# Performance work log

Measured on AMD Instinct MI355X. Metric: run time of the kernel, lower is better.

## Reference

```python
import jax, jax.numpy as jnp
import numpy as np

N, D, Q, V = 16384, 128, 16384, 64

def setup_inputs() -> dict:
    key = jax.random.key(0)
    k1, k2, k3 = jax.random.split(key, 3)
    points = jax.random.normal(k1, (N, D), dtype=jnp.float32)
    values = jax.random.normal(k2, (N, V), dtype=jnp.float32)
    points_q = jax.random.normal(k3, (Q, D), dtype=jnp.float32)
    return {"points": points, "values": values, "points_q": points_q}

def reference(points, values, points_q):
    # Squared Euclidean distances via GEMM form: |q|^2 - 2 q.p + |p|^2  -> [Q, N]
    q_sq = jnp.sum(points_q * points_q, axis=-1, keepdims=True)          # [Q, 1]
    p_sq = jnp.sum(points * points, axis=-1)                             # [N]
    dist2 = q_sq - 2.0 * jnp.einsum('qd,nd->qn', points_q, points) + p_sq
    nn_idx = jnp.argmin(dist2, axis=-1)                                  # [Q]
    return values[nn_idx]                                                # [Q, V]
```

## Files before the change

### kernel.cpp

```cpp
#include <hip/hip_runtime.h>

#define N_PTS 16384
#define DIMS  128
#define NQ    16384
#define NV    64
#define KT2   256
#define BK    64
#define BM    128
#define BN    128
#define CHUNK_NT 16
#define CHUNK_N  (BN * CHUNK_NT)
#define NCHUNK   (N_PTS / CHUNK_N)

typedef __attribute__((ext_vector_type(8))) _Float16 half8;
typedef __attribute__((ext_vector_type(4))) _Float16 half4;
typedef __attribute__((ext_vector_type(4))) float    f32x4;

#define QBLOCKS (NQ * DIMS / 1024)
#define PBLOCKS (N_PTS * DIMS / 1024)
__global__ __launch_bounds__(256) void split_fused(const float* __restrict__ q,
                                                   const float* __restrict__ pts,
                                                   _Float16* __restrict__ Aq,
                                                   _Float16* __restrict__ Bp,
                                                   float* __restrict__ p_sq,
                                                   unsigned long long* __restrict__ keys) {
    int t = blockIdx.x * 256 + threadIdx.x;
    if (t < NQ) keys[t] = ~0ull;
    const float* src;
    _Float16* dst;
    int t2;
    bool is_p = blockIdx.x >= QBLOCKS;
    if (is_p) { t2 = t - QBLOCKS * 256; src = pts; dst = Bp; }
    else      { t2 = t;                 src = q;   dst = Aq; }
    int idx4 = t2 * 4;
    int r = idx4 >> 7, c = idx4 & 127;
    float4 x = *(const float4*)(src + idx4);
    float xs[4] = {x.x, x.y, x.z, x.w};
    half4 h1, h2;
    float s = 0.f;
#pragma unroll
    for (int j = 0; j < 4; ++j) {
        _Float16 a = (_Float16)xs[j];
        h1[j] = a;
        h2[j] = (_Float16)(xs[j] - (float)a);
        s += xs[j] * xs[j];
    }
    _Float16* o = dst + (size_t)r * KT2 + c;
    *(half4*)o = h1; *(half4*)(o + 128) = h2;
    if (is_p) {
#pragma unroll
        for (int off = 1; off < 32; off <<= 1) s += __shfl_xor(s, off, 64);
        if ((threadIdx.x & 31) == 0) p_sq[r] = s;
    }
}

__device__ __forceinline__ unsigned int f2sortable(float f) {
    unsigned int b = __float_as_uint(f);
    return (b & 0x80000000u) ? ~b : (b | 0x80000000u);
}

__device__ __forceinline__ void gload16(const _Float16* g, const _Float16* l) {
    __builtin_amdgcn_global_load_lds((const __attribute__((address_space(1))) void*)g,
                                     (__attribute__((address_space(3))) void*)l, 16, 0, 0);
}

__global__ __launch_bounds__(256, 2) void nn_mfma(const _Float16* __restrict__ A,
                                                  const _Float16* __restrict__ B,
                                                  const float* __restrict__ p_sq,
                                                  unsigned long long* __restrict__ keys) {
    __shared__ _Float16 Ah1[2][BM * BK];
    __shared__ _Float16 Bsl[3][BN * BK];

    const int bid   = blockIdx.x;
    const int mtile = bid >> 3;
    const int chunk = bid & 7;
    const int nbase = chunk * CHUNK_N;

    const int tid = threadIdx.x;
    const int w   = tid >> 6;
    const int l   = tid & 63;
    const int wq  = w >> 1;
    const int wp  = w & 1;
    const int q16 = l >> 4;
    const int c16 = l & 15;

    const int srow = l >> 3;
    const int gch  = (l & 7) ^ (srow & 7);

    const _Float16* __restrict__ pa = A + (size_t)mtile * BM * KT2;
    const _Float16* __restrict__ pb = B + (size_t)nbase * KT2;

    int blane[4], ldsoff[4];
#pragma unroll
    for (int i = 0; i < 4; ++i) {
        blane[i]  = (w * 32 + i * 8 + srow) * KT2 + gch * 8;
        ldsoff[i] = (w * 32 + i * 8) * BK;
    }

    auto stageTo = [&](const _Float16* gbase, _Float16* lbase) {
#pragma unroll
        for (int i = 0; i < 4; ++i)
            gload16(gbase + blane[i], lbase + ldsoff[i]);
    };

    stageTo(pa,      &Ah1[0][0]);
    stageTo(pa + 64, &Ah1[1][0]);
    stageTo(pb,      &Bsl[0][0]);

    half8 ah2[2][2][4];
#pragma unroll
    for (int s = 0; s < 2; ++s)
#pragma unroll
        for (int ks = 0; ks < 2; ++ks)
#pragma unroll
            for (int mi = 0; mi < 4; ++mi) {
                int row = wq * 64 + mi * 16 + c16;
                ah2[s][ks][mi] = *(const half8*)(pa + (size_t)row * KT2 + 128 + s * 64 + ks * 32 + q16 * 8);
            }

    float    best[4][4];
    unsigned bpak[4][2];
#pragma unroll
    for (int mi = 0; mi < 4; ++mi) {
        best[mi][0] = best[mi][1] = best[mi][2] = best[mi][3] = 3.4e38f;
        bpak[mi][0] = bpak[mi][1] = 0;
    }

    f32x4 acc[4][4] = {};

    auto segDual = [&](const _Float16* ah, const half8 (&ar)[2][4], const _Float16* bs) {
#pragma unroll
        for (int ks = 0; ks < 2; ++ks) {
            int slot8 = ((ks * 4 + q16) ^ (c16 & 7)) * 8;
            half8 a[4], b[4];
#pragma unroll
            for (int ni = 0; ni < 4; ++ni)
                b[ni] = *(const half8*)(bs + (wp * 64 + ni * 16 + c16) * BK + slot8);
#pragma unroll
            for (int mi = 0; mi < 4; ++mi)
                a[mi] = *(const half8*)(ah + (wq * 64 + mi * 16 + c16) * BK + slot8);
#pragma unroll
            for (int mi = 0; mi < 4; ++mi)
#pragma unroll
                for (int ni = 0; ni < 4; ++ni)
                    acc[mi][ni] = __builtin_amdgcn_mfma_f32_16x16x32_f16(a[mi], b[ni], acc[mi][ni], 0, 0, 0);
#pragma unroll
            for (int mi = 0; mi < 4; ++mi)
#pragma unroll
                for (int ni = 0; ni < 4; ++ni)
                    acc[mi][ni] = __builtin_amdgcn_mfma_f32_16x16x32_f16(ar[ks][mi], b[ni], acc[mi][ni], 0, 0, 0);
        }
    };
    auto segOne = [&](const _Float16* ah, const _Float16* bs) {
#pragma unroll
        for (int ks = 0; ks < 2; ++ks) {
            int slot8 = ((ks * 4 + q16) ^ (c16 & 7)) * 8;
            half8 a[4], b[4];
#pragma unroll
            for (int ni = 0; ni < 4; ++ni)
                b[ni] = *(const half8*)(bs + (wp * 64 + ni * 16 + c16) * BK + slot8);
#pragma unroll
            for (int mi = 0; mi < 4; ++mi)
                a[mi] = *(const half8*)(ah + (wq * 64 + mi * 16 + c16) * BK + slot8);
#pragma unroll
            for (int mi = 0; mi < 4; ++mi)
#pragma unroll
                for (int ni = 0; ni < 4; ++ni)
                    acc[mi][ni] = __builtin_amdgcn_mfma_f32_16x16x32_f16(a[mi], b[ni], acc[mi][ni], 0, 0, 0);
        }
    };

    _Float16* p0 = &Bsl[0][0];
    _Float16* p1 = &Bsl[1][0];
    _Float16* p2 = &Bsl[2][0];

#pragma unroll 1
    for (int nt = 0; nt < CHUNK_NT; ++nt) {
        const _Float16* pbn = pb + (size_t)nt * BN * KT2;

        float psq[4];
#pragma unroll
        for (int ni = 0; ni < 4; ++ni)
            psq[ni] = p_sq[nbase + nt * BN + wp * 64 + ni * 16 + c16];

        __syncthreads();
        stageTo(pbn + 64, p1);
        segDual(&Ah1[0][0], ah2[0], p0);

        __syncthreads();
        stageTo(pbn + 128, p2);
        stageTo(pbn + 192, p0);
        segDual(&Ah1[1][0], ah2[1], p1);

        __syncthreads();
        if (nt + 1 < CHUNK_NT)
            stageTo(pbn + BN * KT2, p1);
        segOne(&Ah1[0][0], p2);
        segOne(&Ah1[1][0], p0);

        _Float16* t0 = p0;
        p0 = p1; p1 = p2; p2 = t0;

#pragma unroll
        for (int mi = 0; mi < 4; ++mi)
#pragma unroll
            for (int reg = 0; reg < 4; ++reg) {
                float s0 = psq[0] - 2.0f * acc[mi][0][reg];
                float s1 = psq[1] - 2.0f * acc[mi][1][reg];
                float s2 = psq[2] - 2.0f * acc[mi][2][reg];
                float s3 = psq[3] - 2.0f * acc[mi][3][reg];
                float bv = s0; int bn2 = 0;
                if (s1 < bv) { bv = s1; bn2 = 1; }
                if (s2 < bv) { bv = s2; bn2 = 2; }
                if (s3 < bv) { bv = s3; bn2 = 3; }
                bool take = bv < best[mi][reg];
                unsigned lidx = (unsigned)(nt * BN + wp * 64 + (bn2 << 4) + c16);
                unsigned sh = (reg & 1) * 16;
                unsigned cur = bpak[mi][reg >> 1];
                unsigned nw  = (cur & ~(0xFFFFu << sh)) | (lidx << sh);
                best[mi][reg]      = take ? bv : best[mi][reg];
                bpak[mi][reg >> 1] = take ? nw : cur;
            }
#pragma unroll
        for (int mi = 0; mi < 4; ++mi)
#pragma unroll
            for (int ni = 0; ni < 4; ++ni)
                acc[mi][ni] = (f32x4)(0.f);
    }

#pragma unroll
    for (int mi = 0; mi < 4; ++mi)
#pragma unroll
        for (int reg = 0; reg < 4; ++reg) {
            float    bv   = best[mi][reg];
            unsigned lidx = (bpak[mi][reg >> 1] >> ((reg & 1) * 16)) & 0xFFFFu;
#pragma unroll
            for (int off = 1; off < 16; off <<= 1) {
                float    ov = __shfl_xor(bv, off, 64);
                unsigned oi = __shfl_xor((int)lidx, off, 64);
                if (ov < bv || (ov == bv && oi < lidx)) { bv = ov; lidx = oi; }
            }
            if (c16 == 0) {
                int row = mtile * BM + wq * 64 + mi * 16 + q16 * 4 + reg;
                unsigned long long key =
                    ((unsigned long long)f2sortable(bv) << 32) | (unsigned)(nbase + lidx);
                atomicMin(&keys[row], key);
            }
        }
}

__global__ __launch_bounds__(256) void gather_kernel(const unsigned long long* __restrict__ keys,
                                                     const float* __restrict__ values,
                                                     float* __restrict__ out) {
    int tid = threadIdx.x;
    int q = blockIdx.x * 16 + (tid >> 4);
    int c = tid & 15;
    int idx = (int)(keys[q] & 0xFFFFFFFFull);
    const float4* src = (const float4*)(values + (size_t)idx * NV);
    float4*       dst = (float4*)(out + (size_t)q * NV);
    dst[c] = src[c];
}

#define QT 64
#define PT 64
#define LSTRIDE 132
__global__ __launch_bounds__(256, 2) void nn_kernel(const float* __restrict__ points,
                                                    const float* __restrict__ values,
                                                    const float* __restrict__ pointsq,
                                                    const float* __restrict__ p_sq,
                                                    float* __restrict__ out) {
    __shared__ float lq[QT * LSTRIDE];
    __shared__ float lp[PT * LSTRIDE];
    __shared__ float lps[PT];
    __shared__ float red_val[QT][16];
    __shared__ int   red_idx[QT][16];
    __shared__ int   nn_idx[QT];

    const int tid = threadIdx.x;
    const int tx = tid & 15, ty = tid >> 4;
    const int qbase = blockIdx.x * QT;
    {
        int ql = tid >> 2, quad = tid & 3;
        const float4* src = (const float4*)(pointsq + (size_t)(qbase + ql) * DIMS);
#pragma unroll
        for (int j = 0; j < 8; ++j)
            *(float4*)(lq + ql * LSTRIDE + (quad + 4 * j) * 4) = src[quad + 4 * j];
    }
    float minv[4]; int mini[4];
#pragma unroll
    for (int qi = 0; qi < 4; ++qi) { minv[qi] = 3.4e38f; mini[qi] = 0; }
    for (int tile = 0; tile < N_PTS / PT; ++tile) {
        __syncthreads();
        {
            int pl = tid >> 2, quad = tid & 3;
            const float4* src = (const float4*)(points + (size_t)(tile * PT + pl) * DIMS);
#pragma unroll
            for (int j = 0; j < 8; ++j)
                *(float4*)(lp + pl * LSTRIDE + (quad + 4 * j) * 4) = src[quad + 4 * j];
            if (tid < PT) lps[tid] = p_sq[tile * PT + tid];
        }
        __syncthreads();
        float accl[4][4];
#pragma unroll
        for (int qi = 0; qi < 4; ++qi)
#pragma unroll
            for (int pi = 0; pi < 4; ++pi) accl[qi][pi] = 0.f;
        for (int kc = 0; kc < DIMS / 4; ++kc) {
            float4 aq[4], ap[4];
#pragma unroll
            for (int qi = 0; qi < 4; ++qi) aq[qi] = *(const float4*)(lq + (ty + 16 * qi) * LSTRIDE + kc * 4);
#pragma unroll
            for (int pi = 0; pi < 4; ++pi) ap[pi] = *(const float4*)(lp + (tx + 16 * pi) * LSTRIDE + kc * 4);
#pragma unroll
            for (int qi = 0; qi < 4; ++qi)
#pragma unroll
                for (int pi = 0; pi < 4; ++pi) {
                    accl[qi][pi] += aq[qi].x * ap[pi].x; accl[qi][pi] += aq[qi].y * ap[pi].y;
                    accl[qi][pi] += aq[qi].z * ap[pi].z; accl[qi][pi] += aq[qi].w * ap[pi].w;
                }
        }
#pragma unroll
        for (int qi = 0; qi < 4; ++qi)
#pragma unroll
            for (int pi = 0; pi < 4; ++pi) {
                float score = lps[tx + 16 * pi] - 2.f * accl[qi][pi];
                int idx = tile * PT + tx + 16 * pi;
                if (score < minv[qi]) { minv[qi] = score; mini[qi] = idx; }
            }
    }
    __syncthreads();
#pragma unroll
    for (int qi = 0; qi < 4; ++qi) { red_val[ty + 16 * qi][tx] = minv[qi]; red_idx[ty + 16 * qi][tx] = mini[qi]; }
    __syncthreads();
    if (tid < QT) {
        float bv = red_val[tid][0]; int bi = red_idx[tid][0];
#pragma unroll
        for (int t = 1; t < 16; ++t) {
            float v = red_val[tid][t]; int i = red_idx[tid][t];
            if (v < bv || (v == bv && i < bi)) { bv = v; bi = i; }
        }
        nn_idx[tid] = bi;
    }
    __syncthreads();
    {
        int ql = tid >> 2, quad = tid & 3;
        const float4* src = (const float4*)(values + (size_t)nn_idx[ql] * NV);
        float4* dst = (float4*)(out + (size_t)(qbase + ql) * NV);
#pragma unroll
        for (int j = 0; j < 4; ++j) dst[quad * 4 + j] = src[quad * 4 + j];
    }
}

__global__ __launch_bounds__(256) void psq_kernel(const float* __restrict__ points,
                                                  float* __restrict__ p_sq) {
    int row  = blockIdx.x * 4 + (threadIdx.x >> 6);
    int lane = threadIdx.x & 63;
    float2 v = *(const float2*)(points + row * DIMS + lane * 2);
    float s = v.x * v.x + v.y * v.y;
#pragma unroll
    for (int off = 32; off > 0; off >>= 1) s += __shfl_xor(s, off, 64);
    if (lane == 0) p_sq[row] = s;
}

extern "C" void kernel_launch(void* const* d_in, const int* in_sizes, int n_in,
                              void* d_out, int out_size, void* d_ws, size_t ws_size,
                              hipStream_t stream) {
    const float* points  = (const float*)d_in[0];
    const float* values  = (const float*)d_in[1];
    const float* pointsq = (const float*)d_in[2];
    float*       out     = (float*)d_out;

    const size_t OFF_KEYS = 0;
    const size_t OFF_PSQ  = 131072;
    const size_t OFF_A    = 196608;
    const size_t OFF_B    = OFF_A + (size_t)NQ * KT2 * 2;
    const size_t NEEDED   = OFF_B + (size_t)N_PTS * KT2 * 2;

    if (ws_size >= NEEDED) {
        unsigned long long* keys = (unsigned long long*)((char*)d_ws + OFF_KEYS);
        float*    p_sq = (float*)((char*)d_ws + OFF_PSQ);
        _Float16* Aq   = (_Float16*)((char*)d_ws + OFF_A);
        _Float16* Bp   = (_Float16*)((char*)d_ws + OFF_B);

        split_fused<<<QBLOCKS + PBLOCKS, 256, 0, stream>>>(pointsq, points, Aq, Bp, p_sq, keys);
        nn_mfma<<<(NQ / BM) * NCHUNK, 256, 0, stream>>>(Aq, Bp, p_sq, keys);
        gather_kernel<<<NQ / 16, 256, 0, stream>>>(keys, values, out);
    } else {
        float* p_sq = (float*)d_ws;
        psq_kernel<<<N_PTS / 4, 256, 0, stream>>>(points, p_sq);
        nn_kernel<<<NQ / QT, 256, 0, stream>>>(points, values, pointsq, p_sq, out);
    }
}
```

Baseline: 256.6 us.

## Hold second A k-slice in registers and use four fixed B LDS slots

After: 342.1 us. 33.3% more time.

```diff
diff --git a/kernel.cpp b/kernel.cpp
--- a/kernel.cpp
+++ b/kernel.cpp
@@ -68,8 +68,8 @@
                                                   const _Float16* __restrict__ B,
                                                   const float* __restrict__ p_sq,
                                                   unsigned long long* __restrict__ keys) {
-    __shared__ _Float16 Ah1[2][BM * BK];
-    __shared__ _Float16 Bsl[3][BN * BK];
+    __shared__ _Float16 Ah1[BM * BK];
+    __shared__ _Float16 Bsl[4][BN * BK];
 
     const int bid   = blockIdx.x;
     const int mtile = bid >> 3;
@@ -103,20 +103,22 @@
             gload16(gbase + blane[i], lbase + ldsoff[i]);
     };
 
-    stageTo(pa,      &Ah1[0][0]);
-    stageTo(pa + 64, &Ah1[1][0]);
+    stageTo(pa,      &Ah1[0]);
     stageTo(pb,      &Bsl[0][0]);
-
+    stageTo(pb + 64, &Bsl[1][0]);
+
+    half8 ah1b[2][4];
     half8 ah2[2][2][4];
 #pragma unroll
-    for (int s = 0; s < 2; ++s)
-#pragma unroll
-        for (int ks = 0; ks < 2; ++ks)
-#pragma unroll
-            for (int mi = 0; mi < 4; ++mi) {
-                int row = wq * 64 + mi * 16 + c16;
+    for (int ks = 0; ks < 2; ++ks)
+#pragma unroll
+        for (int mi = 0; mi < 4; ++mi) {
+            int row = wq * 64 + mi * 16 + c16;
+            ah1b[ks][mi] = *(const half8*)(pa + (size_t)row * KT2 + 64 + ks * 32 + q16 * 8);
+#pragma unroll
+            for (int s = 0; s < 2; ++s)
                 ah2[s][ks][mi] = *(const half8*)(pa + (size_t)row * KT2 + 128 + s * 64 + ks * 32 + q16 * 8);
-            }
+        }
 
     float    best[4][4];
     unsigned bpak[4][2];
@@ -128,7 +130,7 @@
 
     f32x4 acc[4][4] = {};
 
-    auto segDual = [&](const _Float16* ah, const half8 (&ar)[2][4], const _Float16* bs) {
+    auto segDualL = [&](const _Float16* ah, const half8 (&ar)[2][4], const _Float16* bs) {
 #pragma unroll
         for (int ks = 0; ks < 2; ++ks) {
             int slot8 = ((ks * 4 + q16) ^ (c16 & 7)) * 8;
@@ -151,7 +153,27 @@
                     acc[mi][ni] = __builtin_amdgcn_mfma_f32_16x16x32_f16(ar[ks][mi], b[ni], acc[mi][ni], 0, 0, 0);
         }
     };
-    auto segOne = [&](const _Float16* ah, const _Float16* bs) {
+    auto segDualR = [&](const half8 (&a0)[2][4], const half8 (&a1)[2][4], const _Float16* bs) {
+#pragma unroll
+        for (int ks = 0; ks < 2; ++ks) {
+            int slot8 = ((ks * 4 + q16) ^ (c16 & 7)) * 8;
+            half8 b[4];
+#pragma unroll
+            for (int ni = 0; ni < 4; ++ni)
+                b[ni] = *(const half8*)(bs + (wp * 64 + ni * 16 + c16) * BK + slot8);
+#pragma unroll
+            for (int mi = 0; mi < 4; ++mi)
+#pragma unroll
+                for (int ni = 0; ni < 4; ++ni)
+                    acc[mi][ni] = __builtin_amdgcn_mfma_f32_16x16x32_f16(a0[ks][mi], b[ni], acc[mi][ni], 0, 0, 0);
+#pragma unroll
+            for (int mi = 0; mi < 4; ++mi)
+#pragma unroll
+                for (int ni = 0; ni < 4; ++ni)
+                    acc[mi][ni] = __builtin_amdgcn_mfma_f32_16x16x32_f16(a1[ks][mi], b[ni], acc[mi][ni], 0, 0, 0);
+        }
+    };
+    auto segOneL = [&](const _Float16* ah, const _Float16* bs) {
 #pragma unroll
         for (int ks = 0; ks < 2; ++ks) {
             int slot8 = ((ks * 4 + q16) ^ (c16 & 7)) * 8;
@@ -169,14 +191,26 @@
                     acc[mi][ni] = __builtin_amdgcn_mfma_f32_16x16x32_f16(a[mi], b[ni], acc[mi][ni], 0, 0, 0);
         }
     };
-
-    _Float16* p0 = &Bsl[0][0];
-    _Float16* p1 = &Bsl[1][0];
-    _Float16* p2 = &Bsl[2][0];
+    auto segOneR = [&](const half8 (&a0)[2][4], const _Float16* bs) {
+#pragma unroll
+        for (int ks = 0; ks < 2; ++ks) {
+            int slot8 = ((ks * 4 + q16) ^ (c16 & 7)) * 8;
+            half8 b[4];
+#pragma unroll
+            for (int ni = 0; ni < 4; ++ni)
+                b[ni] = *(const half8*)(bs + (wp * 64 + ni * 16 + c16) * BK + slot8);
+#pragma unroll
+            for (int mi = 0; mi < 4; ++mi)
+#pragma unroll
+                for (int ni = 0; ni < 4; ++ni)
+                    acc[mi][ni] = __builtin_amdgcn_mfma_f32_16x16x32_f16(a0[ks][mi], b[ni], acc[mi][ni], 0, 0, 0);
+        }
+    };
 
 #pragma unroll 1
     for (int nt = 0; nt < CHUNK_NT; ++nt) {
         const _Float16* pbn = pb + (size_t)nt * BN * KT2;
+        const bool more = (nt + 1 < CHUNK_NT);
 
         float psq[4];
 #pragma unroll
@@ -184,22 +218,18 @@
             psq[ni] = p_sq[nbase + nt * BN + wp * 64 + ni * 16 + c16];
 
         __syncthreads();
-        stageTo(pbn + 64, p1);
-        segDual(&Ah1[0][0], ah2[0], p0);
+        stageTo(pbn + 128, &Bsl[2][0]);
+        stageTo(pbn + 192, &Bsl[3][0]);
+        segDualL(&Ah1[0], ah2[0], &Bsl[0][0]);
 
         __syncthreads();
-        stageTo(pbn + 128, p2);
-        stageTo(pbn + 192, p0);
-        segDual(&Ah1[1][0], ah2[1], p1);
+        if (more) stageTo(pbn + BN * KT2, &Bsl[0][0]);
+        segDualR(ah1b, ah2[1], &Bsl[1][0]);
 
         __syncthreads();
-        if (nt + 1 < CHUNK_NT)
-            stageTo(pbn + BN * KT2, p1);
-        segOne(&Ah1[0][0], p2);
-        segOne(&Ah1[1][0], p0);
-
-        _Float16* t0 = p0;
-        p0 = p1; p1 = p2; p2 = t0;
+        if (more) stageTo(pbn + BN * KT2 + 64, &Bsl[1][0]);
+        segOneL(&Ah1[0], &Bsl[2][0]);
+        segOneR(ah1b, &Bsl[3][0]);
 
 #pragma unroll
         for (int mi = 0; mi < 4; ++mi)
```

## Halve query tile to 64 rows, double-buffer B, raise occupancy to 3 blocks

Applied to the files above, without the earlier changes.

Measured after the change: 265.6 us. 1.04x slower.

```diff
diff --git a/kernel.cpp b/kernel.cpp
--- a/kernel.cpp
+++ b/kernel.cpp
@@ -6,7 +6,7 @@
 #define NV    64
 #define KT2   256
 #define BK    64
-#define BM    128
+#define BM    64
 #define BN    128
 #define CHUNK_NT 16
 #define CHUNK_N  (BN * CHUNK_NT)
@@ -64,12 +64,12 @@
                                      (__attribute__((address_space(3))) void*)l, 16, 0, 0);
 }
 
-__global__ __launch_bounds__(256, 2) void nn_mfma(const _Float16* __restrict__ A,
+__global__ __launch_bounds__(256, 3) void nn_mfma(const _Float16* __restrict__ A,
                                                   const _Float16* __restrict__ B,
                                                   const float* __restrict__ p_sq,
                                                   unsigned long long* __restrict__ keys) {
     __shared__ _Float16 Ah1[2][BM * BK];
-    __shared__ _Float16 Bsl[3][BN * BK];
+    __shared__ _Float16 Bsl[2][BN * BK];
 
     const int bid   = blockIdx.x;
     const int mtile = bid >> 3;
@@ -90,62 +90,73 @@
     const _Float16* __restrict__ pa = A + (size_t)mtile * BM * KT2;
     const _Float16* __restrict__ pb = B + (size_t)nbase * KT2;
 
-    int blane[4], ldsoff[4];
+    int blane[4], ldsoffB[4];
 #pragma unroll
     for (int i = 0; i < 4; ++i) {
-        blane[i]  = (w * 32 + i * 8 + srow) * KT2 + gch * 8;
-        ldsoff[i] = (w * 32 + i * 8) * BK;
-    }
-
-    auto stageTo = [&](const _Float16* gbase, _Float16* lbase) {
+        blane[i]   = (w * 32 + i * 8 + srow) * KT2 + gch * 8;
+        ldsoffB[i] = (w * 32 + i * 8) * BK;
+    }
+    int alane[2], ldsoffA[2];
+#pragma unroll
+    for (int i = 0; i < 2; ++i) {
+        alane[i]   = (w * 16 + i * 8 + srow) * KT2 + gch * 8;
+        ldsoffA[i] = (w * 16 + i * 8) * BK;
+    }
+
+    auto stageB = [&](const _Float16* gbase, _Float16* lbase) {
 #pragma unroll
         for (int i = 0; i < 4; ++i)
-            gload16(gbase + blane[i], lbase + ldsoff[i]);
+            gload16(gbase + blane[i], lbase + ldsoffB[i]);
     };
-
-    stageTo(pa,      &Ah1[0][0]);
-    stageTo(pa + 64, &Ah1[1][0]);
-    stageTo(pb,      &Bsl[0][0]);
-
-    half8 ah2[2][2][4];
+    auto stageA = [&](const _Float16* gbase, _Float16* lbase) {
+#pragma unroll
+        for (int i = 0; i < 2; ++i)
+            gload16(gbase + alane[i], lbase + ldsoffA[i]);
+    };
+
+    stageA(pa,      &Ah1[0][0]);
+    stageA(pa + 64, &Ah1[1][0]);
+    stageB(pb,      &Bsl[0][0]);
+
+    half8 ah2[2][2][2];
 #pragma unroll
     for (int s = 0; s < 2; ++s)
 #pragma unroll
         for (int ks = 0; ks < 2; ++ks)
 #pragma unroll
-            for (int mi = 0; mi < 4; ++mi) {
-                int row = wq * 64 + mi * 16 + c16;
+            for (int mi = 0; mi < 2; ++mi) {
+                int row = wq * 32 + mi * 16 + c16;
                 ah2[s][ks][mi] = *(const half8*)(pa + (size_t)row * KT2 + 128 + s * 64 + ks * 32 + q16 * 8);
             }
 
-    float    best[4][4];
-    unsigned bpak[4][2];
-#pragma unroll
-    for (int mi = 0; mi < 4; ++mi) {
+    float    best[2][4];
+    unsigned bpak[2][2];
+#pragma unroll
+    for (int mi = 0; mi < 2; ++mi) {
         best[mi][0] = best[mi][1] = best[mi][2] = best[mi][3] = 3.4e38f;
         bpak[mi][0] = bpak[mi][1] = 0;
     }
 
-    f32x4 acc[4][4] = {};
-
-    auto segDual = [&](const _Float16* ah, const half8 (&ar)[2][4], const _Float16* bs) {
+    f32x4 acc[2][4] = {};
+
+    auto segDual = [&](const _Float16* ah, const half8 (&ar)[2][2], const _Float16* bs) {
 #pragma unroll
         for (int ks = 0; ks < 2; ++ks) {
             int slot8 = ((ks * 4 + q16) ^ (c16 & 7)) * 8;
-            half8 a[4], b[4];
+            half8 a[2], b[4];
 #pragma unroll
             for (int ni = 0; ni < 4; ++ni)
                 b[ni] = *(const half8*)(bs + (wp * 64 + ni * 16 + c16) * BK + slot8);
 #pragma unroll
-            for (int mi = 0; mi < 4; ++mi)
-                a[mi] = *(const half8*)(ah + (wq * 64 + mi * 16 + c16) * BK + slot8);
-#pragma unroll
-            for (int mi = 0; mi < 4; ++mi)
+            for (int mi = 0; mi < 2; ++mi)
+                a[mi] = *(const half8*)(ah + (wq * 32 + mi * 16 + c16) * BK + slot8);
+#pragma unroll
+            for (int mi = 0; mi < 2; ++mi)
 #pragma unroll
                 for (int ni = 0; ni < 4; ++ni)
                     acc[mi][ni] = __builtin_amdgcn_mfma_f32_16x16x32_f16(a[mi], b[ni], acc[mi][ni], 0, 0, 0);
 #pragma unroll
-            for (int mi = 0; mi < 4; ++mi)
+            for (int mi = 0; mi < 2; ++mi)
 #pragma unroll
                 for (int ni = 0; ni < 4; ++ni)
                     acc[mi][ni] = __builtin_amdgcn_mfma_f32_16x16x32_f16(ar[ks][mi], b[ni], acc[mi][ni], 0, 0, 0);
@@ -155,24 +166,20 @@
 #pragma unroll
         for (int ks = 0; ks < 2; ++ks) {
             int slot8 = ((ks * 4 + q16) ^ (c16 & 7)) * 8;
-            half8 a[4], b[4];
+            half8 a[2], b[4];
 #pragma unroll
             for (int ni = 0; ni < 4; ++ni)
                 b[ni] = *(const half8*)(bs + (wp * 64 + ni * 16 + c16) * BK + slot8);
 #pragma unroll
-            for (int mi = 0; mi < 4; ++mi)
-                a[mi] = *(const half8*)(ah + (wq * 64 + mi * 16 + c16) * BK + slot8);
-#pragma unroll
-            for (int mi = 0; mi < 4; ++mi)
+            for (int mi = 0; mi < 2; ++mi)
+                a[mi] = *(const half8*)(ah + (wq * 32 + mi * 16 + c16) * BK + slot8);
+#pragma unroll
+            for (int mi = 0; mi < 2; ++mi)
 #pragma unroll
                 for (int ni = 0; ni < 4; ++ni)
                     acc[mi][ni] = __builtin_amdgcn_mfma_f32_16x16x32_f16(a[mi], b[ni], acc[mi][ni], 0, 0, 0);
         }
     };
-
-    _Float16* p0 = &Bsl[0][0];
-    _Float16* p1 = &Bsl[1][0];
-    _Float16* p2 = &Bsl[2][0];
 
 #pragma unroll 1
     for (int nt = 0; nt < CHUNK_NT; ++nt) {
@@ -184,25 +191,24 @@
             psq[ni] = p_sq[nbase + nt * BN + wp * 64 + ni * 16 + c16];
 
         __syncthreads();
-        stageTo(pbn + 64, p1);
-        segDual(&Ah1[0][0], ah2[0], p0);
-
-        __syncthreads();
-        stageTo(pbn + 128, p2);
-        stageTo(pbn + 192, p0);
-        segDual(&Ah1[1][0], ah2[1], p1);
+        stageB(pbn + 64, &Bsl[1][0]);
+        segDual(&Ah1[0][0], ah2[0], &Bsl[0][0]);
+
+        __syncthreads();
+        stageB(pbn + 128, &Bsl[0][0]);
+        segDual(&Ah1[1][0], ah2[1], &Bsl[1][0]);
+
+        __syncthreads();
+        stageB(pbn + 192, &Bsl[1][0]);
+        segOne(&Ah1[0][0], &Bsl[0][0]);
 
         __syncthreads();
         if (nt + 1 < CHUNK_NT)
-            stageTo(pbn + BN * KT2, p1);
-        segOne(&Ah1[0][0], p2);
-        segOne(&Ah1[1][0], p0);
-
-        _Float16* t0 = p0;
-        p0 = p1; p1 = p2; p2 = t0;
-
-#pragma unroll
-        for (int mi = 0; mi < 4; ++mi)
+            stageB(pbn + BN * KT2, &Bsl[0][0]);
+        segOne(&Ah1[1][0], &Bsl[1][0]);
+
+#pragma unroll
+        for (int mi = 0; mi < 2; ++mi)
 #pragma unroll
             for (int reg = 0; reg < 4; ++reg) {
                 float s0 = psq[0] - 2.0f * acc[mi][0][reg];
@@ -222,14 +228,14 @@
                 bpak[mi][reg >> 1] = take ? nw : cur;
             }
 #pragma unroll
-        for (int mi = 0; mi < 4; ++mi)
+        for (int mi = 0; mi < 2; ++mi)
 #pragma unroll
             for (int ni = 0; ni < 4; ++ni)
                 acc[mi][ni] = (f32x4)(0.f);
     }
 
 #pragma unroll
-    for (int mi = 0; mi < 4; ++mi)
+    for (int mi = 0; mi < 2; ++mi)
 #pragma unroll
         for (int reg = 0; reg < 4; ++reg) {
             float    bv   = best[mi][reg];
@@ -241,7 +247,7 @@
                 if (ov < bv || (ov == bv && oi < lidx)) { bv = ov; lidx = oi; }
             }
             if (c16 == 0) {
-                int row = mtile * BM + wq * 64 + mi * 16 + q16 * 4 + reg;
+                int row = mtile * BM + wq * 32 + mi * 16 + q16 * 4 + reg;
                 unsigned long long key =
                     ((unsigned long long)f2sortable(bv) << 32) | (unsigned)(nbase + lidx);
                 atomicMin(&keys[row], key);
```
